# Performance work log

Hardware: AMD Instinct MI355X
Metric: run time of the kernel (lower is better)

## Reference

```python
import jax, jax.numpy as jnp
import numpy as np

N_NODES = 10000
N_EDGES = 160000
IN_CH = 1030
HID = 256
HEADS = 4
OUT_CH = 49
NEG_SLOPE = 0.2
EPS = 1e-5


def setup_inputs() -> dict:
    key = jax.random.key(0)
    ks = jax.random.split(key, 20)
    HC = HID * HEADS  # 1024
    inp = {
        "x": jax.random.normal(ks[0], (N_NODES, IN_CH), dtype=jnp.float32),
        "edge_index": jax.random.randint(ks[1], (2, N_EDGES), 0, N_NODES, dtype=jnp.int64),
        # conv1 (GATv2): lin_l (source), lin_r (target), att, out bias
        "c1_wl": jax.random.normal(ks[2], (IN_CH, HC), dtype=jnp.float32) * 0.03,
        "c1_bl": jnp.zeros((HC,), dtype=jnp.float32),
        "c1_wr": jax.random.normal(ks[3], (IN_CH, HC), dtype=jnp.float32) * 0.03,
        "c1_br": jnp.zeros((HC,), dtype=jnp.float32),
        "c1_att": jax.random.normal(ks[4], (HEADS, HID), dtype=jnp.float32) * 0.06,
        "c1_bias": jnp.zeros((HC,), dtype=jnp.float32),
        # norm1 (per-node LayerNorm over channels)
        "ln1_w": jnp.ones((HC,), dtype=jnp.float32),
        "ln1_b": jnp.zeros((HC,), dtype=jnp.float32),
        # conv2
        "c2_wl": jax.random.normal(ks[5], (HC, HC), dtype=jnp.float32) * 0.03,
        "c2_bl": jnp.zeros((HC,), dtype=jnp.float32),
        "c2_wr": jax.random.normal(ks[6], (HC, HC), dtype=jnp.float32) * 0.03,
        "c2_br": jnp.zeros((HC,), dtype=jnp.float32),
        "c2_att": jax.random.normal(ks[7], (HEADS, HID), dtype=jnp.float32) * 0.06,
        "c2_bias": jnp.zeros((HC,), dtype=jnp.float32),
        # norm2
        "ln2_w": jnp.ones((HC,), dtype=jnp.float32),
        "ln2_b": jnp.zeros((HC,), dtype=jnp.float32),
        # classifier: Linear(HC, HID) -> ELU -> Linear(HID, OUT_CH)
        "cls_w1": jax.random.normal(ks[8], (HC, HID), dtype=jnp.float32) * 0.03,
        "cls_b1": jnp.zeros((HID,), dtype=jnp.float32),
        "cls_w2": jax.random.normal(ks[9], (HID, OUT_CH), dtype=jnp.float32) * 0.06,
        "cls_b2": jnp.zeros((OUT_CH,), dtype=jnp.float32),
    }
    return inp


def gatv2_conv(x, src, dst, wl, bl, wr, br, att, bias, n_nodes):
    """PyG GATv2Conv, concat heads. src/dst include self loops."""
    H, C = att.shape
    xl = (x @ wl + bl).reshape(-1, H, C)  # source transform [N,H,C]
    xr = (x @ wr + br).reshape(-1, H, C)  # target transform [N,H,C]
    m = xl[src] + xr[dst]                  # [E,H,C] gather + add
    e = jnp.einsum("ehc,hc->eh", jax.nn.leaky_relu(m, NEG_SLOPE), att)  # [E,H]
    # segment softmax over destination node
    emax = jax.ops.segment_max(e, dst, num_segments=n_nodes)
    p = jnp.exp(e - emax[dst])
    denom = jax.ops.segment_sum(p, dst, num_segments=n_nodes)
    alpha = p / (denom[dst] + 1e-16)       # [E,H]
    out = jax.ops.segment_sum(xl[src] * alpha[:, :, None], dst, num_segments=n_nodes)
    return out.reshape(n_nodes, H * C) + bias


def layer_norm(x, w, b):
    mu = jnp.mean(x, axis=-1, keepdims=True)
    var = jnp.var(x, axis=-1, keepdims=True)
    return (x - mu) / jnp.sqrt(var + EPS) * w + b


def reference(x, edge_index, c1_wl, c1_bl, c1_wr, c1_br, c1_att, c1_bias,
              ln1_w, ln1_b, c2_wl, c2_bl, c2_wr, c2_br, c2_att, c2_bias,
              ln2_w, ln2_b, cls_w1, cls_b1, cls_w2, cls_b2):
    n = x.shape[0]
    loops = jnp.arange(n, dtype=edge_index.dtype)
    src = jnp.concatenate([edge_index[0], loops])  # add_self_loops=True
    dst = jnp.concatenate([edge_index[1], loops])

    h = gatv2_conv(x, src, dst, c1_wl, c1_bl, c1_wr, c1_br, c1_att, c1_bias, n)
    h = jax.nn.elu(layer_norm(h, ln1_w, ln1_b))
    # dropout: identity at inference
    h = gatv2_conv(h, src, dst, c2_wl, c2_bl, c2_wr, c2_br, c2_att, c2_bias, n)
    h = jax.nn.elu(layer_norm(h, ln2_w, ln2_b))
    h = jax.nn.elu(h @ cls_w1 + cls_b1)
    return h @ cls_w2 + cls_b2  # [N, 49]
```

## Files before the change

kernel.cpp:

```cpp
#include <hip/hip_runtime.h>
#include <stdint.h>

#define N_NODES 10000
#define N_EDGES 160000
#define E_TOT   170000
#define IN_CH   1030
#define HC      1024
#define OUT_CH  49
#define NEG_SLOPE 0.2f
#define LN_EPS 1e-5f
#define LOG2E 1.4426950408889634f

#define MPAD  10112
#define K1PAD 1088

typedef __attribute__((ext_vector_type(8))) __bf16 bf16x8;
typedef __attribute__((ext_vector_type(4))) float floatx4;
typedef __attribute__((ext_vector_type(2))) float floatx2;
typedef _Float16 h2 __attribute__((ext_vector_type(2)));

static __device__ __forceinline__ unsigned short f2bf(float f) {
  union { float f; uint32_t u; } v; v.f = f;
  uint32_t u = v.u;
  u += 0x7fffu + ((u >> 16) & 1u);
  return (unsigned short)(u >> 16);
}
static __device__ __forceinline__ unsigned short f2h(float f) {
  _Float16 h = (_Float16)f;
  union { _Float16 h; unsigned short u; } v; v.h = h; return v.u;
}
static __device__ __forceinline__ h2 bits2h2(uint32_t u) {
  union { uint32_t i; h2 h; } v; v.i = u; return v.h;
}
static __device__ __forceinline__ floatx2 h2f2(h2 a) {
  floatx2 r; r.x = (float)a.x; r.y = (float)a.y; return r;
}

static __device__ __forceinline__ float wred_add(float x) {
#define DPP_ADD(ctrl, rmask)                                                   \
  x += __builtin_bit_cast(float, __builtin_amdgcn_update_dpp(                  \
           0, __builtin_bit_cast(int, x), ctrl, rmask, 0xf, true))
  DPP_ADD(0x111, 0xf);
  DPP_ADD(0x112, 0xf);
  DPP_ADD(0x114, 0xf);
  DPP_ADD(0x118, 0xf);
  DPP_ADD(0x142, 0xa);
  DPP_ADD(0x143, 0xc);
#undef DPP_ADD
  return __builtin_bit_cast(float,
      __builtin_amdgcn_readlane(__builtin_bit_cast(int, x), 63));
}


__global__ void cast_x_kernel(const float* __restrict__ x, unsigned short* __restrict__ xa,
                              int* __restrict__ counts) {
  int idx = blockIdx.x * 256 + threadIdx.x;
  if (idx < N_NODES) counts[idx] = 0;
  if (idx >= N_NODES * K1PAD) return;
  int m = idx / K1PAD, k = idx - m * K1PAD;
  float v = (k < IN_CH) ? x[m * IN_CH + k] : 0.f;
  xa[idx] = f2bf(v);
}

static __device__ __forceinline__ void transpose_body(
    float (*tile)[33], const float* __restrict__ wa, const float* __restrict__ wb,
    int split, int lda, int ldb, int Kvalid, int Kout,
    unsigned short* __restrict__ out, int bx, int by, int t) {
  int n0 = bx * 32, k0 = by * 32;
  int tx = t & 31, ty = t >> 5;
#pragma unroll
  for (int i = 0; i < 4; i++) {
    int k = k0 + ty + i * 8;
    int n = n0 + tx;
    float v = 0.f;
    if (k < Kvalid) v = (n < split) ? wa[(size_t)k * lda + n] : wb[(size_t)k * ldb + (n - split)];
    tile[ty + i * 8][tx] = v;
  }
  __syncthreads();
#pragma unroll
  for (int i = 0; i < 4; i++) {
    int n = n0 + ty + i * 8;
    int k = k0 + tx;
    out[(size_t)n * Kout + k] = f2bf(tile[tx][ty + i * 8]);
  }
}

#define NB_W1 2176
#define NB_W2 2048
#define NB_WC 256
#define NB_CNT 665
__global__ __launch_bounds__(256) void prep2_kernel(
    const float* __restrict__ c1_wl, const float* __restrict__ c1_wr,
    const float* __restrict__ c2_wl, const float* __restrict__ c2_wr,
    const float* __restrict__ cls_w1,
    const int* __restrict__ dstArr, int* __restrict__ counts,
    unsigned short* __restrict__ wt1, unsigned short* __restrict__ wt2,
    unsigned short* __restrict__ wtc1)
{
  __shared__ float tile[32][33];
  int b = blockIdx.x, t = threadIdx.x;
  if (b < NB_W1) {
    transpose_body(tile, c1_wl, c1_wr, 1024, 1024, 1024, IN_CH, K1PAD, wt1, b & 63, b >> 6, t);
  } else if (b < NB_W1 + NB_W2) {
    int bb = b - NB_W1;
    transpose_body(tile, c2_wl, c2_wr, 1024, 1024, 1024, 1024, 1024, wt2, bb & 63, bb >> 6, t);
  } else if (b < NB_W1 + NB_W2 + NB_WC) {
    int bb = b - (NB_W1 + NB_W2);
    transpose_body(tile, cls_w1, cls_w1, 256, 256, 256, 1024, 1024, wtc1, bb & 7, bb >> 3, t);
  } else {
    int e = (b - (NB_W1 + NB_W2 + NB_WC)) * 256 + t;
    if (e < E_TOT) {
      int d = (e < N_EDGES) ? dstArr[e] : (e - N_EDGES);
      atomicAdd(&counts[d], 1);
    }
  }
}

__global__ __launch_bounds__(256) void scan_kernel(const int* __restrict__ counts,
                                                   int* __restrict__ rstart,
                                                   int* __restrict__ rwork) {
  __shared__ int sm[256];
  int t = threadIdx.x;
  int b0 = t * 40;
  int b1 = b0 + 40; if (b1 > N_NODES) b1 = N_NODES; if (b0 > N_NODES) b0 = N_NODES;
  int s = 0;
  for (int i = b0; i < b1; i++) s += counts[i];
  sm[t] = s; __syncthreads();
  for (int st = 1; st < 256; st <<= 1) {
    int add = (t >= st) ? sm[t - st] : 0;
    __syncthreads();
    sm[t] += add;
    __syncthreads();
  }
  int run = sm[t] - s;
  for (int i = b0; i < b1; i++) { rstart[i] = run; rwork[i] = run; run += counts[i]; }
  if (t == 255) rstart[N_NODES] = run;
}

__global__ void scatter_kernel(const int* __restrict__ srcArr, const int* __restrict__ dstArr,
                               int* __restrict__ rwork, int* __restrict__ csrsrc) {
  int e = blockIdx.x * 256 + threadIdx.x;
  if (e >= E_TOT) return;
  int d, sv;
  if (e < N_EDGES) { d = dstArr[e]; sv = srcArr[e]; }
  else { d = e - N_EDGES; sv = d; }
  int pos = atomicAdd(&rwork[d], 1);
  csrsrc[pos] = sv;
}

template <int MODE, int KC>
__global__ __launch_bounds__(256, 4) void gemm_bf16(
    const unsigned short* __restrict__ A, const unsigned short* __restrict__ Bt,
    float* __restrict__ Cf, unsigned short* __restrict__ Cb,
    const float* __restrict__ blo, const float* __restrict__ bhi,
    int M, int ldc, int bsplit)
{
  __shared__ __align__(16) unsigned short As[128 * 64];
  __shared__ __align__(16) unsigned short Bs[128 * 64];
  const int t = threadIdx.x;
  const int w = t >> 6, lane = t & 63;

  const unsigned int nwg = gridDim.x * gridDim.y;
  const unsigned int bid = blockIdx.y * gridDim.x + blockIdx.x;
  const unsigned int q8 = nwg >> 3, r8 = nwg & 7;
  const unsigned int xcd = bid & 7, sub = bid >> 3;
  const unsigned int wg = (xcd < r8 ? xcd * (q8 + 1) : r8 * (q8 + 1) + (xcd - r8) * q8) + sub;
  const int tile_n = (wg % gridDim.x) * 128, tile_m = (wg / gridDim.x) * 128;

  floatx4 acc[4][4] = {};

  const int qq = w * 64 + lane;
  const int row0 = qq >> 3;
  const int gj = (qq & 7) ^ (row0 & 7);
  const unsigned short* gA0 = A  + (size_t)(tile_m + row0) * KC + gj * 8;
  const unsigned short* gB0 = Bt + (size_t)(tile_n + row0) * KC + gj * 8;

  const int wm = (w >> 1) * 64, wn = (w & 1) * 64;
  const int lrow = lane & 15, cg0 = (lane >> 4);
  const int sw = lrow & 7;

#pragma unroll 1
  for (int k0 = 0; k0 < KC; k0 += 64) {
#pragma unroll
    for (int p = 0; p < 4; p++) {
      __builtin_amdgcn_global_load_lds(
          (const __attribute__((address_space(1))) void*)(gA0 + p * 32 * KC),
          (__attribute__((address_space(3))) void*)(As + p * 2048 + w * 512), 16, 0, 0);
      __builtin_amdgcn_global_load_lds(
          (const __attribute__((address_space(1))) void*)(gB0 + p * 32 * KC),
          (__attribute__((address_space(3))) void*)(Bs + p * 2048 + w * 512), 16, 0, 0);
    }
    gA0 += 64; gB0 += 64;
    __syncthreads();
#pragma unroll
    for (int h = 0; h < 2; h++) {
      const int sc = (h * 4 + cg0) ^ sw;
      bf16x8 a[4], b[4];
#pragma unroll
      for (int mi = 0; mi < 4; mi++)
        a[mi] = *(const bf16x8*)(As + (wm + mi * 16 + lrow) * 64 + sc * 8);
#pragma unroll
      for (int ni = 0; ni < 4; ni++)
        b[ni] = *(const bf16x8*)(Bs + (wn + ni * 16 + lrow) * 64 + sc * 8);
#pragma unroll
      for (int mi = 0; mi < 4; mi++)
#pragma unroll
        for (int ni = 0; ni < 4; ni++)
          acc[mi][ni] = __builtin_amdgcn_mfma_f32_16x16x32_bf16(a[mi], b[ni], acc[mi][ni], 0, 0, 0);
    }
    __syncthreads();
  }

  const int rbase = (lane >> 4) * 4;
#pragma unroll
  for (int mi = 0; mi < 4; mi++) {
#pragma unroll
    for (int r = 0; r < 4; r++) {
      int m = tile_m + wm + mi * 16 + rbase + r;
      if (m >= M) continue;
#pragma unroll
      for (int ni = 0; ni < 4; ni++) {
        int n = tile_n + wn + ni * 16 + lrow;
        float v = acc[mi][ni][r] + (n < bsplit ? blo[n] : bhi[n - bsplit]);
        if (MODE == 0) {
          Cf[(size_t)m * ldc + n] = v;
        } else if (MODE == 1) {
          Cf[(size_t)m * ldc + n] = v > 0.f ? v : expm1f(v);
        } else {
          Cb[(size_t)m * 2048 + n] = f2h(v);
        }
      }
    }
  }
}


__global__ __launch_bounds__(256) void gat_ln_kernel(
    const unsigned short* __restrict__ xlr,
    const float* __restrict__ att,
    const int* __restrict__ csrsrc, const int* __restrict__ rstart,
    const float* __restrict__ bias,
    const float* __restrict__ lnw, const float* __restrict__ lnb,
    unsigned short* __restrict__ out)
{
  const int d = blockIdx.x;
  const int t = threadIdx.x;
  const int lane = t & 63, wv = t >> 6;
  const int c = wv * 256 + lane * 4;

  uint2 xru = *(const uint2*)(xlr + (size_t)d * 2048 + 1024 + c);
  h2 xr0 = bits2h2(xru.x), xr1 = bits2h2(xru.y);
  float4 aw4 = *(const float4*)(att + c);
  h2 aw0, aw1;
  aw0.x = (_Float16)(aw4.x * LOG2E); aw0.y = (_Float16)(aw4.y * LOG2E);
  aw1.x = (_Float16)(aw4.z * LOG2E); aw1.y = (_Float16)(aw4.w * LOG2E);
  const h2 ns = {(_Float16)NEG_SLOPE, (_Float16)NEG_SLOPE};
  const unsigned short* xbase = xlr + c;

  const int start = rstart[d], end = rstart[d + 1];
  const int last = end - 1;
  const int ngroups = (end - start + 3) >> 2;

  float m = -3.0e38f, l = 0.f;
  floatx2 accA = {0.f, 0.f}, accB = {0.f, 0.f};

#define CIDX(e) csrsrc[(e) < last ? (e) : last]
  int sA0 = CIDX(start),     sA1 = CIDX(start + 1);
  int sA2 = CIDX(start + 2), sA3 = CIDX(start + 3);
  uint2 uA0 = *(const uint2*)(xbase + (size_t)sA0 * 2048);
  uint2 uA1 = *(const uint2*)(xbase + (size_t)sA1 * 2048);
  uint2 uA2 = *(const uint2*)(xbase + (size_t)sA2 * 2048);
  uint2 uA3 = *(const uint2*)(xbase + (size_t)sA3 * 2048);
  int sB0 = CIDX(start + 4), sB1 = CIDX(start + 5);
  int sB2 = CIDX(start + 6), sB3 = CIDX(start + 7);

  for (int g = 0; g < ngroups; g++) {
    const int base = start + (g << 2);
    int sC0 = CIDX(base + 8),  sC1 = CIDX(base + 9);
    int sC2 = CIDX(base + 10), sC3 = CIDX(base + 11);
    uint2 uB0 = *(const uint2*)(xbase + (size_t)sB0 * 2048);
    uint2 uB1 = *(const uint2*)(xbase + (size_t)sB1 * 2048);
    uint2 uB2 = *(const uint2*)(xbase + (size_t)sB2 * 2048);
    uint2 uB3 = *(const uint2*)(xbase + (size_t)sB3 * 2048);

    h2 xh0a = bits2h2(uA0.x), xh0b = bits2h2(uA0.y);
    h2 xh1a = bits2h2(uA1.x), xh1b = bits2h2(uA1.y);
    h2 xh2a = bits2h2(uA2.x), xh2b = bits2h2(uA2.y);
    h2 xh3a = bits2h2(uA3.x), xh3b = bits2h2(uA3.y);
    h2 t0a = xh0a + xr0, t0b = xh0b + xr1;
    h2 t1a = xh1a + xr0, t1b = xh1b + xr1;
    h2 t2a = xh2a + xr0, t2b = xh2b + xr1;
    h2 t3a = xh3a + xr0, t3b = xh3b + xr1;
    h2 r0a = __builtin_elementwise_max(t0a, t0a * ns);
    h2 r0b = __builtin_elementwise_max(t0b, t0b * ns);
    h2 r1a = __builtin_elementwise_max(t1a, t1a * ns);
    h2 r1b = __builtin_elementwise_max(t1b, t1b * ns);
    h2 r2a = __builtin_elementwise_max(t2a, t2a * ns);
    h2 r2b = __builtin_elementwise_max(t2b, t2b * ns);
    h2 r3a = __builtin_elementwise_max(t3a, t3a * ns);
    h2 r3b = __builtin_elementwise_max(t3b, t3b * ns);
    float p0 = __builtin_amdgcn_fdot2(r0b, aw1, __builtin_amdgcn_fdot2(r0a, aw0, 0.f, false), false);
    float p1 = __builtin_amdgcn_fdot2(r1b, aw1, __builtin_amdgcn_fdot2(r1a, aw0, 0.f, false), false);
    float p2 = __builtin_amdgcn_fdot2(r2b, aw1, __builtin_amdgcn_fdot2(r2a, aw0, 0.f, false), false);
    float p3 = __builtin_amdgcn_fdot2(r3b, aw1, __builtin_amdgcn_fdot2(r3a, aw0, 0.f, false), false);
    p0 = wred_add(p0);
    p1 = wred_add(p1);
    p2 = wred_add(p2);
    p3 = wred_add(p3);
    float mx = fmaxf(fmaxf(p0, p1), fmaxf(p2, p3));
    if (mx > m) {
      float sc = exp2f(m - mx);
      floatx2 scv; scv.x = sc; scv.y = sc;
      accA *= scv; accB *= scv; l *= sc;
      m = mx;
    }
    float pe0 = exp2f(p0 - m);
    float pe1 = (base + 1 <= last) ? exp2f(p1 - m) : 0.f;
    float pe2 = (base + 2 <= last) ? exp2f(p2 - m) : 0.f;
    float pe3 = (base + 3 <= last) ? exp2f(p3 - m) : 0.f;
    floatx2 x0A = h2f2(xh0a), x0B = h2f2(xh0b);
    floatx2 x1A = h2f2(xh1a), x1B = h2f2(xh1b);
    floatx2 x2A = h2f2(xh2a), x2B = h2f2(xh2b);
    floatx2 x3A = h2f2(xh3a), x3B = h2f2(xh3b);
    floatx2 v0; v0.x = pe0; v0.y = pe0;
    floatx2 v1; v1.x = pe1; v1.y = pe1;
    floatx2 v2; v2.x = pe2; v2.y = pe2;
    floatx2 v3; v3.x = pe3; v3.y = pe3;
    accA += x0A * v0; accA += x1A * v1; accA += x2A * v2; accA += x3A * v3;
    accB += x0B * v0; accB += x1B * v1; accB += x2B * v2; accB += x3B * v3;
    l += pe0 + pe1 + pe2 + pe3;

    uA0 = uB0; uA1 = uB1; uA2 = uB2; uA3 = uB3;
    sB0 = sC0; sB1 = sC1; sB2 = sC2; sB3 = sC3;
  }
#undef CIDX

  float rd = 1.f / (l + 1e-16f);
  float4 bv = *(const float4*)(bias + c);
  float o0 = accA.x * rd + bv.x, o1 = accA.y * rd + bv.y;
  float o2 = accB.x * rd + bv.z, o3 = accB.y * rd + bv.w;

  __shared__ float ws1[4], ws2[4];
  float s1 = o0 + o1 + o2 + o3;
  float s2 = o0 * o0 + o1 * o1 + o2 * o2 + o3 * o3;
#pragma unroll
  for (int mm = 32; mm >= 1; mm >>= 1) {
    s1 += __shfl_xor(s1, mm, 64);
    s2 += __shfl_xor(s2, mm, 64);
  }
  if (lane == 0) { ws1[wv] = s1; ws2[wv] = s2; }
  __syncthreads();
  float mean = (ws1[0] + ws1[1] + ws1[2] + ws1[3]) * (1.f / 1024.f);
  float var  = (ws2[0] + ws2[1] + ws2[2] + ws2[3]) * (1.f / 1024.f) - mean * mean;
  float rstd = rsqrtf(var + LN_EPS);
  float4 wv4 = *(const float4*)(lnw + c);
  float4 bb  = *(const float4*)(lnb + c);
  float z0 = (o0 - mean) * rstd * wv4.x + bb.x; z0 = z0 > 0.f ? z0 : expm1f(z0);
  float z1 = (o1 - mean) * rstd * wv4.y + bb.y; z1 = z1 > 0.f ? z1 : expm1f(z1);
  float z2 = (o2 - mean) * rstd * wv4.z + bb.z; z2 = z2 > 0.f ? z2 : expm1f(z2);
  float z3 = (o3 - mean) * rstd * wv4.w + bb.w; z3 = z3 > 0.f ? z3 : expm1f(z3);
  ushort4 u;
  u.x = f2bf(z0); u.y = f2bf(z1); u.z = f2bf(z2); u.w = f2bf(z3);
  *(ushort4*)(out + (size_t)d * 1024 + c) = u;
}


__global__ __launch_bounds__(64) void cls2_kernel(
    const float* __restrict__ h3, const float* __restrict__ w2,
    const float* __restrict__ b2, float* __restrict__ out)
{
  __shared__ float row[256];
  int node = blockIdx.x, t = threadIdx.x;
  *(float4*)(row + t * 4) = *(const float4*)(h3 + (size_t)node * 256 + t * 4);
  __syncthreads();
  if (t < OUT_CH) {
    float a0 = 0.f, a1 = 0.f, a2 = 0.f, a3 = 0.f;
#pragma unroll 4
    for (int k = 0; k < 256; k += 4) {
      float4 r = *(const float4*)(row + k);
      a0 += r.x * w2[(k + 0) * OUT_CH + t];
      a1 += r.y * w2[(k + 1) * OUT_CH + t];
      a2 += r.z * w2[(k + 2) * OUT_CH + t];
      a3 += r.w * w2[(k + 3) * OUT_CH + t];
    }
    out[node * OUT_CH + t] = (a0 + a1) + (a2 + a3) + b2[t];
  }
}


extern "C" void kernel_launch(void* const* d_in, const int* in_sizes, int n_in,
                              void* d_out, int out_size, void* d_ws, size_t ws_size,
                              hipStream_t stream)
{
  const float* x       = (const float*)d_in[0];
  const int*   ei      = (const int*)d_in[1];
  const float* c1_wl   = (const float*)d_in[2];
  const float* c1_bl   = (const float*)d_in[3];
  const float* c1_wr   = (const float*)d_in[4];
  const float* c1_br   = (const float*)d_in[5];
  const float* c1_att  = (const float*)d_in[6];
  const float* c1_bias = (const float*)d_in[7];
  const float* ln1_w   = (const float*)d_in[8];
  const float* ln1_b   = (const float*)d_in[9];
  const float* c2_wl   = (const float*)d_in[10];
  const float* c2_bl   = (const float*)d_in[11];
  const float* c2_wr   = (const float*)d_in[12];
  const float* c2_br   = (const float*)d_in[13];
  const float* c2_att  = (const float*)d_in[14];
  const float* c2_bias = (const float*)d_in[15];
  const float* ln2_w   = (const float*)d_in[16];
  const float* ln2_b   = (const float*)d_in[17];
  const float* cls_w1  = (const float*)d_in[18];
  const float* cls_b1  = (const float*)d_in[19];
  const float* cls_w2  = (const float*)d_in[20];
  const float* cls_b2  = (const float*)d_in[21];

  const int* srcArr = ei;
  const int* dstArr = ei + N_EDGES;

  char* ws = (char*)d_ws;
  size_t off = 0;
  auto alloc = [&](size_t bytes) { void* p = ws + off; off += (bytes + 255) & ~(size_t)255; return p; };
  unsigned short* xa      = (unsigned short*)alloc((size_t)MPAD * K1PAD * 2);
  unsigned short* wt1     = (unsigned short*)alloc((size_t)2048 * K1PAD * 2);
  unsigned short* wt2     = (unsigned short*)alloc((size_t)2048 * 1024 * 2);
  unsigned short* wtc1    = (unsigned short*)alloc((size_t)256 * 1024 * 2);
  unsigned short* xlr     = (unsigned short*)alloc((size_t)N_NODES * 2048 * 2);
  float*          h3      = (float*)alloc((size_t)N_NODES * 256 * 4);
  unsigned short* hb      = (unsigned short*)alloc((size_t)MPAD * 1024 * 2);
  int*            counts  = (int*)alloc(N_NODES * 4);
  int*            rwork   = (int*)alloc(N_NODES * 4);
  int*            rstart  = (int*)alloc((N_NODES + 1) * 4);
  int*            csrsrc  = (int*)alloc(E_TOT * 4);
  (void)in_sizes; (void)n_in; (void)out_size; (void)ws_size;

  cast_x_kernel<<<(N_NODES * K1PAD + 255) / 256, 256, 0, stream>>>(x, xa, counts);
  prep2_kernel<<<NB_W1 + NB_W2 + NB_WC + NB_CNT, 256, 0, stream>>>(
      c1_wl, c1_wr, c2_wl, c2_wr, cls_w1, dstArr, counts, wt1, wt2, wtc1);

  scan_kernel<<<1, 256, 0, stream>>>(counts, rstart, rwork);
  scatter_kernel<<<(E_TOT + 255) / 256, 256, 0, stream>>>(srcArr, dstArr, rwork, csrsrc);

  gemm_bf16<2, K1PAD><<<dim3(16, 79), 256, 0, stream>>>(xa, wt1, nullptr, xlr, c1_bl, c1_br, N_NODES, 0, 1024);
  gat_ln_kernel<<<N_NODES, 256, 0, stream>>>(xlr, c1_att, csrsrc, rstart, c1_bias, ln1_w, ln1_b, hb);

  gemm_bf16<2, 1024><<<dim3(16, 79), 256, 0, stream>>>(hb, wt2, nullptr, xlr, c2_bl, c2_br, N_NODES, 0, 1024);
  gat_ln_kernel<<<N_NODES, 256, 0, stream>>>(xlr, c2_att, csrsrc, rstart, c2_bias, ln2_w, ln2_b, hb);

  gemm_bf16<1, 1024><<<dim3(2, 79), 256, 0, stream>>>(hb, wtc1, h3, nullptr, cls_b1, cls_b1, N_NODES, 256, 1024);
  cls2_kernel<<<N_NODES, 64, 0, stream>>>(h3, cls_w2, cls_b2, (float*)d_out);
}
```

Measured before the change: 498.3 us.

## Split GAT edge loop into two independent online-softmax streams with deeper prefetch

The per-node GATv2 aggregation loop now interleaves two independent groups of four edges, each with its own running max, sum and accumulators, merged after the loop. Leftover edges are handled by a scalar tail loop. The CSR index array is padded with zeros so prefetch reads past the end stay in bounds without clamping. The intent is to double the gathers in flight and shorten the dependency chain through the softmax rescale. The cost is more registers, a merge step, and wasted gather loads for padded or out-of-range prefetches.

```diff
diff --git a/kernel.cpp b/kernel.cpp
--- a/kernel.cpp
+++ b/kernel.cpp
@@ -49,6 +49,57 @@
 #undef DPP_ADD
   return __builtin_bit_cast(float,
       __builtin_amdgcn_readlane(__builtin_bit_cast(int, x), 63));
+}
+
+static __device__ __forceinline__ void group4(
+    uint2 u0, uint2 u1, uint2 u2, uint2 u3,
+    h2 xr0, h2 xr1, h2 aw0, h2 aw1, h2 ns,
+    float& m, float& l, floatx2& acc0, floatx2& acc1)
+{
+  h2 xh0a = bits2h2(u0.x), xh0b = bits2h2(u0.y);
+  h2 xh1a = bits2h2(u1.x), xh1b = bits2h2(u1.y);
+  h2 xh2a = bits2h2(u2.x), xh2b = bits2h2(u2.y);
+  h2 xh3a = bits2h2(u3.x), xh3b = bits2h2(u3.y);
+  h2 t0a = xh0a + xr0, t0b = xh0b + xr1;
+  h2 t1a = xh1a + xr0, t1b = xh1b + xr1;
+  h2 t2a = xh2a + xr0, t2b = xh2b + xr1;
+  h2 t3a = xh3a + xr0, t3b = xh3b + xr1;
+  h2 r0a = __builtin_elementwise_max(t0a, t0a * ns);
+  h2 r0b = __builtin_elementwise_max(t0b, t0b * ns);
+  h2 r1a = __builtin_elementwise_max(t1a, t1a * ns);
+  h2 r1b = __builtin_elementwise_max(t1b, t1b * ns);
+  h2 r2a = __builtin_elementwise_max(t2a, t2a * ns);
+  h2 r2b = __builtin_elementwise_max(t2b, t2b * ns);
+  h2 r3a = __builtin_elementwise_max(t3a, t3a * ns);
+  h2 r3b = __builtin_elementwise_max(t3b, t3b * ns);
+  float p0 = __builtin_amdgcn_fdot2(r0b, aw1, __builtin_amdgcn_fdot2(r0a, aw0, 0.f, false), false);
+  float p1 = __builtin_amdgcn_fdot2(r1b, aw1, __builtin_amdgcn_fdot2(r1a, aw0, 0.f, false), false);
+  float p2 = __builtin_amdgcn_fdot2(r2b, aw1, __builtin_amdgcn_fdot2(r2a, aw0, 0.f, false), false);
+  float p3 = __builtin_amdgcn_fdot2(r3b, aw1, __builtin_amdgcn_fdot2(r3a, aw0, 0.f, false), false);
+  p0 = wred_add(p0);
+  p1 = wred_add(p1);
+  p2 = wred_add(p2);
+  p3 = wred_add(p3);
+  float mx = fmaxf(fmaxf(p0, p1), fmaxf(p2, p3));
+  if (mx > m) {
+    float sc = exp2f(m - mx);
+    floatx2 scv; scv.x = sc; scv.y = sc;
+    acc0 *= scv; acc1 *= scv; l *= sc;
+    m = mx;
+  }
+  float pe0 = exp2f(p0 - m), pe1 = exp2f(p1 - m);
+  float pe2 = exp2f(p2 - m), pe3 = exp2f(p3 - m);
+  floatx2 x0A = h2f2(xh0a), x0B = h2f2(xh0b);
+  floatx2 x1A = h2f2(xh1a), x1B = h2f2(xh1b);
+  floatx2 x2A = h2f2(xh2a), x2B = h2f2(xh2b);
+  floatx2 x3A = h2f2(xh3a), x3B = h2f2(xh3b);
+  floatx2 v0; v0.x = pe0; v0.y = pe0;
+  floatx2 v1; v1.x = pe1; v1.y = pe1;
+  floatx2 v2; v2.x = pe2; v2.y = pe2;
+  floatx2 v3; v3.x = pe3; v3.y = pe3;
+  acc0 += x0A * v0; acc0 += x1A * v1; acc0 += x2A * v2; acc0 += x3A * v3;
+  acc1 += x0B * v0; acc1 += x1B * v1; acc1 += x2B * v2; acc1 += x3B * v3;
+  l += pe0 + pe1 + pe2 + pe3;
 }
 
 
@@ -141,6 +192,7 @@
                                int* __restrict__ rwork, int* __restrict__ csrsrc) {
   int e = blockIdx.x * 256 + threadIdx.x;
   if (e >= E_TOT) return;
+  if (e < 32) csrsrc[E_TOT + e] = 0;
   int d, sv;
   if (e < N_EDGES) { d = dstArr[e]; sv = srcArr[e]; }
   else { d = e - N_EDGES; sv = d; }
@@ -258,82 +310,79 @@
   const unsigned short* xbase = xlr + c;
 
   const int start = rstart[d], end = rstart[d + 1];
-  const int last = end - 1;
-  const int ngroups = (end - start + 3) >> 2;
-
-  float m = -3.0e38f, l = 0.f;
-  floatx2 accA = {0.f, 0.f}, accB = {0.f, 0.f};
-
-#define CIDX(e) csrsrc[(e) < last ? (e) : last]
-  int sA0 = CIDX(start),     sA1 = CIDX(start + 1);
-  int sA2 = CIDX(start + 2), sA3 = CIDX(start + 3);
-  uint2 uA0 = *(const uint2*)(xbase + (size_t)sA0 * 2048);
-  uint2 uA1 = *(const uint2*)(xbase + (size_t)sA1 * 2048);
-  uint2 uA2 = *(const uint2*)(xbase + (size_t)sA2 * 2048);
-  uint2 uA3 = *(const uint2*)(xbase + (size_t)sA3 * 2048);
-  int sB0 = CIDX(start + 4), sB1 = CIDX(start + 5);
-  int sB2 = CIDX(start + 6), sB3 = CIDX(start + 7);
-
-  for (int g = 0; g < ngroups; g++) {
-    const int base = start + (g << 2);
-    int sC0 = CIDX(base + 8),  sC1 = CIDX(base + 9);
-    int sC2 = CIDX(base + 10), sC3 = CIDX(base + 11);
-    uint2 uB0 = *(const uint2*)(xbase + (size_t)sB0 * 2048);
-    uint2 uB1 = *(const uint2*)(xbase + (size_t)sB1 * 2048);
-    uint2 uB2 = *(const uint2*)(xbase + (size_t)sB2 * 2048);
-    uint2 uB3 = *(const uint2*)(xbase + (size_t)sB3 * 2048);
-
-    h2 xh0a = bits2h2(uA0.x), xh0b = bits2h2(uA0.y);
-    h2 xh1a = bits2h2(uA1.x), xh1b = bits2h2(uA1.y);
-    h2 xh2a = bits2h2(uA2.x), xh2b = bits2h2(uA2.y);
-    h2 xh3a = bits2h2(uA3.x), xh3b = bits2h2(uA3.y);
+  const int ng = (end - start) >> 2;
+  const int nA = (ng + 1) >> 1, nB = ng >> 1;
+
+  float mA = -3.0e38f, lA = 0.f, mB = -3.0e38f, lB = 0.f;
+  floatx2 a0A = {0.f, 0.f}, a1A = {0.f, 0.f};
+  floatx2 a0B = {0.f, 0.f}, a1B = {0.f, 0.f};
+
+  int iA0 = csrsrc[start],     iA1 = csrsrc[start + 1];
+  int iA2 = csrsrc[start + 2], iA3 = csrsrc[start + 3];
+  int iB0 = csrsrc[start + 4], iB1 = csrsrc[start + 5];
+  int iB2 = csrsrc[start + 6], iB3 = csrsrc[start + 7];
+  uint2 uA0 = *(const uint2*)(xbase + (size_t)iA0 * 2048);
+  uint2 uA1 = *(const uint2*)(xbase + (size_t)iA1 * 2048);
+  uint2 uA2 = *(const uint2*)(xbase + (size_t)iA2 * 2048);
+  uint2 uA3 = *(const uint2*)(xbase + (size_t)iA3 * 2048);
+  uint2 uB0 = *(const uint2*)(xbase + (size_t)iB0 * 2048);
+  uint2 uB1 = *(const uint2*)(xbase + (size_t)iB1 * 2048);
+  uint2 uB2 = *(const uint2*)(xbase + (size_t)iB2 * 2048);
+  uint2 uB3 = *(const uint2*)(xbase + (size_t)iB3 * 2048);
+  iA0 = csrsrc[start + 8];  iA1 = csrsrc[start + 9];
+  iA2 = csrsrc[start + 10]; iA3 = csrsrc[start + 11];
+  iB0 = csrsrc[start + 12]; iB1 = csrsrc[start + 13];
+  iB2 = csrsrc[start + 14]; iB3 = csrsrc[start + 15];
+
+  for (int j = 0; j < nA; j++) {
+    const int base = start + (j << 3);
+    group4(uA0, uA1, uA2, uA3, xr0, xr1, aw0, aw1, ns, mA, lA, a0A, a1A);
+    uA0 = *(const uint2*)(xbase + (size_t)iA0 * 2048);
+    uA1 = *(const uint2*)(xbase + (size_t)iA1 * 2048);
+    uA2 = *(const uint2*)(xbase + (size_t)iA2 * 2048);
+    uA3 = *(const uint2*)(xbase + (size_t)iA3 * 2048);
+    iA0 = csrsrc[base + 16]; iA1 = csrsrc[base + 17];
+    iA2 = csrsrc[base + 18]; iA3 = csrsrc[base + 19];
+    if (j < nB)
+      group4(uB0, uB1, uB2, uB3, xr0, xr1, aw0, aw1, ns, mB, lB, a0B, a1B);
+    uB0 = *(const uint2*)(xbase + (size_t)iB0 * 2048);
+    uB1 = *(const uint2*)(xbase + (size_t)iB1 * 2048);
+    uB2 = *(const uint2*)(xbase + (size_t)iB2 * 2048);
+    uB3 = *(const uint2*)(xbase + (size_t)iB3 * 2048);
+    iB0 = csrsrc[base + 20]; iB1 = csrsrc[base + 21];
+    iB2 = csrsrc[base + 22]; iB3 = csrsrc[base + 23];
+  }
+
+  float m = fmaxf(mA, mB);
+  float sA = exp2f(mA - m), sB = exp2f(mB - m);
+  float l = lA * sA + lB * sB;
+  floatx2 vsA; vsA.x = sA; vsA.y = sA;
+  floatx2 vsB; vsB.x = sB; vsB.y = sB;
+  floatx2 accA = a0A * vsA + a0B * vsB;
+  floatx2 accB = a1A * vsA + a1B * vsB;
+
+  for (int i = start + (ng << 2); i < end; i++) {
+    int s0 = csrsrc[i];
+    uint2 u0 = *(const uint2*)(xbase + (size_t)s0 * 2048);
+    h2 xh0a = bits2h2(u0.x), xh0b = bits2h2(u0.y);
     h2 t0a = xh0a + xr0, t0b = xh0b + xr1;
-    h2 t1a = xh1a + xr0, t1b = xh1b + xr1;
-    h2 t2a = xh2a + xr0, t2b = xh2b + xr1;
-    h2 t3a = xh3a + xr0, t3b = xh3b + xr1;
     h2 r0a = __builtin_elementwise_max(t0a, t0a * ns);
     h2 r0b = __builtin_elementwise_max(t0b, t0b * ns);
-    h2 r1a = __builtin_elementwise_max(t1a, t1a * ns);
-    h2 r1b = __builtin_elementwise_max(t1b, t1b * ns);
-    h2 r2a = __builtin_elementwise_max(t2a, t2a * ns);
-    h2 r2b = __builtin_elementwise_max(t2b, t2b * ns);
-    h2 r3a = __builtin_elementwise_max(t3a, t3a * ns);
-    h2 r3b = __builtin_elementwise_max(t3b, t3b * ns);
     float p0 = __builtin_amdgcn_fdot2(r0b, aw1, __builtin_amdgcn_fdot2(r0a, aw0, 0.f, false), false);
-    float p1 = __builtin_amdgcn_fdot2(r1b, aw1, __builtin_amdgcn_fdot2(r1a, aw0, 0.f, false), false);
-    float p2 = __builtin_amdgcn_fdot2(r2b, aw1, __builtin_amdgcn_fdot2(r2a, aw0, 0.f, false), false);
-    float p3 = __builtin_amdgcn_fdot2(r3b, aw1, __builtin_amdgcn_fdot2(r3a, aw0, 0.f, false), false);
     p0 = wred_add(p0);
-    p1 = wred_add(p1);
-    p2 = wred_add(p2);
-    p3 = wred_add(p3);
-    float mx = fmaxf(fmaxf(p0, p1), fmaxf(p2, p3));
-    if (mx > m) {
-      float sc = exp2f(m - mx);
+    if (p0 > m) {
+      float sc = exp2f(m - p0);
       floatx2 scv; scv.x = sc; scv.y = sc;
       accA *= scv; accB *= scv; l *= sc;
-      m = mx;
+      m = p0;
     }
     float pe0 = exp2f(p0 - m);
-    float pe1 = (base + 1 <= last) ? exp2f(p1 - m) : 0.f;
-    float pe2 = (base + 2 <= last) ? exp2f(p2 - m) : 0.f;
-    float pe3 = (base + 3 <= last) ? exp2f(p3 - m) : 0.f;
     floatx2 x0A = h2f2(xh0a), x0B = h2f2(xh0b);
-    floatx2 x1A = h2f2(xh1a), x1B = h2f2(xh1b);
-    floatx2 x2A = h2f2(xh2a), x2B = h2f2(xh2b);
-    floatx2 x3A = h2f2(xh3a), x3B = h2f2(xh3b);
-    floatx2 v0; v0.x = pe0; v0.y = pe0;
-    floatx2 v1; v1.x = pe1; v1.y = pe1;
-    floatx2 v2; v2.x = pe2; v2.y = pe2;
-    floatx2 v3; v3.x = pe3; v3.y = pe3;
-    accA += x0A * v0; accA += x1A * v1; accA += x2A * v2; accA += x3A * v3;
-    accB += x0B * v0; accB += x1B * v1; accB += x2B * v2; accB += x3B * v3;
-    l += pe0 + pe1 + pe2 + pe3;
-
-    uA0 = uB0; uA1 = uB1; uA2 = uB2; uA3 = uB3;
-    sB0 = sC0; sB1 = sC1; sB2 = sC2; sB3 = sC3;
-  }
-#undef CIDX
+    floatx2 pe0v; pe0v.x = pe0; pe0v.y = pe0;
+    accA += x0A * pe0v;
+    accB += x0B * pe0v;
+    l += pe0;
+  }
 
   float rd = 1.f / (l + 1e-16f);
   float4 bv = *(const float4*)(bias + c);
@@ -431,7 +480,7 @@
   int*            counts  = (int*)alloc(N_NODES * 4);
   int*            rwork   = (int*)alloc(N_NODES * 4);
   int*            rstart  = (int*)alloc((N_NODES + 1) * 4);
-  int*            csrsrc  = (int*)alloc(E_TOT * 4);
+  int*            csrsrc  = (int*)alloc((E_TOT + 32) * 4);
   (void)in_sizes; (void)n_in; (void)out_size; (void)ws_size;
 
   cast_x_kernel<<<(N_NODES * K1PAD + 255) / 256, 256, 0, stream>>>(x, xa, counts);
```

Result: no change. 507.3 us (+1.8%).

## Split GAT aggregation per head with head-major layout and separate LayerNorm kernel

Applied to the files above, without the earlier changes.

The GEMM epilogue now writes xl and xr into separate head-major buffers ([head][node][256]). The aggregation kernel is restructured so each block handles one head for four nodes, one node per wave, with the block index swizzled so nearby blocks share a head. Each head's gathered source rows then sit in a compact 5 MB region, which is meant to improve L2 locality for the random neighbor gathers. LayerNorm+ELU moves to a separate kernel that reads an intermediate fp16 buffer, adding one extra launch and a round trip of 20 MB.

```diff
diff --git a/kernel.cpp b/kernel.cpp
--- a/kernel.cpp
+++ b/kernel.cpp
@@ -141,6 +141,7 @@
                                int* __restrict__ rwork, int* __restrict__ csrsrc) {
   int e = blockIdx.x * 256 + threadIdx.x;
   if (e >= E_TOT) return;
+  if (e < 32) csrsrc[E_TOT + e] = 0;
   int d, sv;
   if (e < N_EDGES) { d = dstArr[e]; sv = srcArr[e]; }
   else { d = e - N_EDGES; sv = d; }
@@ -152,6 +153,7 @@
 __global__ __launch_bounds__(256, 4) void gemm_bf16(
     const unsigned short* __restrict__ A, const unsigned short* __restrict__ Bt,
     float* __restrict__ Cf, unsigned short* __restrict__ Cb,
+    unsigned short* __restrict__ Cb2,
     const float* __restrict__ blo, const float* __restrict__ bhi,
     int M, int ldc, int bsplit)
 {
@@ -227,7 +229,9 @@
         } else if (MODE == 1) {
           Cf[(size_t)m * ldc + n] = v > 0.f ? v : expm1f(v);
         } else {
-          Cb[(size_t)m * 2048 + n] = f2h(v);
+          unsigned short* dst = (n < 1024) ? Cb : Cb2;
+          int hh = (n >> 8) & 3, ch = n & 255;
+          dst[((size_t)hh * N_NODES + m) * 256 + ch] = f2h(v);
         }
       }
     }
@@ -235,110 +239,151 @@
 }
 
 
-__global__ __launch_bounds__(256) void gat_ln_kernel(
-    const unsigned short* __restrict__ xlr,
+__global__ __launch_bounds__(256) void gat_head_kernel(
+    const unsigned short* __restrict__ xlh,
+    const unsigned short* __restrict__ xrh,
     const float* __restrict__ att,
     const int* __restrict__ csrsrc, const int* __restrict__ rstart,
     const float* __restrict__ bias,
+    unsigned short* __restrict__ obuf)
+{
+  const int bid = blockIdx.x;
+  const int h = (bid & 7) >> 1;
+  const int g = ((bid >> 3) << 1) | (bid & 1);
+  const int t = threadIdx.x;
+  const int lane = t & 63, wv = t >> 6;
+  const int d = g * 4 + wv;
+  const int c = lane * 4;
+  const size_t hoff = (size_t)h * (N_NODES * 256);
+
+  uint2 xru = *(const uint2*)(xrh + hoff + (size_t)d * 256 + c);
+  h2 xr0 = bits2h2(xru.x), xr1 = bits2h2(xru.y);
+  float4 aw4 = *(const float4*)(att + h * 256 + c);
+  h2 aw0, aw1;
+  aw0.x = (_Float16)(aw4.x * LOG2E); aw0.y = (_Float16)(aw4.y * LOG2E);
+  aw1.x = (_Float16)(aw4.z * LOG2E); aw1.y = (_Float16)(aw4.w * LOG2E);
+  const h2 ns = {(_Float16)NEG_SLOPE, (_Float16)NEG_SLOPE};
+  const unsigned short* xbase = xlh + hoff + c;
+
+  int start = rstart[d], deg = rstart[d + 1] - start;
+
+  float m = -3.0e38f, l = 0.f;
+  floatx2 accA = {0.f, 0.f}, accB = {0.f, 0.f};
+
+  int i = 0;
+  if (deg >= 4) {
+    int sA0 = csrsrc[start],     sA1 = csrsrc[start + 1];
+    int sA2 = csrsrc[start + 2], sA3 = csrsrc[start + 3];
+    uint2 uA0 = *(const uint2*)(xbase + (size_t)sA0 * 256);
+    uint2 uA1 = *(const uint2*)(xbase + (size_t)sA1 * 256);
+    uint2 uA2 = *(const uint2*)(xbase + (size_t)sA2 * 256);
+    uint2 uA3 = *(const uint2*)(xbase + (size_t)sA3 * 256);
+    int sB0 = csrsrc[start + 4], sB1 = csrsrc[start + 5];
+    int sB2 = csrsrc[start + 6], sB3 = csrsrc[start + 7];
+    for (; i + 4 <= deg; i += 4) {
+      int sC0 = csrsrc[start + i + 8],  sC1 = csrsrc[start + i + 9];
+      int sC2 = csrsrc[start + i + 10], sC3 = csrsrc[start + i + 11];
+      uint2 uB0 = *(const uint2*)(xbase + (size_t)sB0 * 256);
+      uint2 uB1 = *(const uint2*)(xbase + (size_t)sB1 * 256);
+      uint2 uB2 = *(const uint2*)(xbase + (size_t)sB2 * 256);
+      uint2 uB3 = *(const uint2*)(xbase + (size_t)sB3 * 256);
+
+      h2 xh0a = bits2h2(uA0.x), xh0b = bits2h2(uA0.y);
+      h2 xh1a = bits2h2(uA1.x), xh1b = bits2h2(uA1.y);
+      h2 xh2a = bits2h2(uA2.x), xh2b = bits2h2(uA2.y);
+      h2 xh3a = bits2h2(uA3.x), xh3b = bits2h2(uA3.y);
+      h2 t0a = xh0a + xr0, t0b = xh0b + xr1;
+      h2 t1a = xh1a + xr0, t1b = xh1b + xr1;
+      h2 t2a = xh2a + xr0, t2b = xh2b + xr1;
+      h2 t3a = xh3a + xr0, t3b = xh3b + xr1;
+      h2 r0a = __builtin_elementwise_max(t0a, t0a * ns);
+      h2 r0b = __builtin_elementwise_max(t0b, t0b * ns);
+      h2 r1a = __builtin_elementwise_max(t1a, t1a * ns);
+      h2 r1b = __builtin_elementwise_max(t1b, t1b * ns);
+      h2 r2a = __builtin_elementwise_max(t2a, t2a * ns);
+      h2 r2b = __builtin_elementwise_max(t2b, t2b * ns);
+      h2 r3a = __builtin_elementwise_max(t3a, t3a * ns);
+      h2 r3b = __builtin_elementwise_max(t3b, t3b * ns);
+      float p0 = __builtin_amdgcn_fdot2(r0b, aw1, __builtin_amdgcn_fdot2(r0a, aw0, 0.f, false), false);
+      float p1 = __builtin_amdgcn_fdot2(r1b, aw1, __builtin_amdgcn_fdot2(r1a, aw0, 0.f, false), false);
+      float p2 = __builtin_amdgcn_fdot2(r2b, aw1, __builtin_amdgcn_fdot2(r2a, aw0, 0.f, false), false);
+      float p3 = __builtin_amdgcn_fdot2(r3b, aw1, __builtin_amdgcn_fdot2(r3a, aw0, 0.f, false), false);
+      p0 = wred_add(p0);
+      p1 = wred_add(p1);
+      p2 = wred_add(p2);
+      p3 = wred_add(p3);
+      float mx = fmaxf(fmaxf(p0, p1), fmaxf(p2, p3));
+      if (mx > m) {
+        float sc = exp2f(m - mx);
+        floatx2 scv; scv.x = sc; scv.y = sc;
+        accA *= scv; accB *= scv; l *= sc;
+        m = mx;
+      }
+      float pe0 = exp2f(p0 - m), pe1 = exp2f(p1 - m);
+      float pe2 = exp2f(p2 - m), pe3 = exp2f(p3 - m);
+      floatx2 x0A = h2f2(xh0a), x0B = h2f2(xh0b);
+      floatx2 x1A = h2f2(xh1a), x1B = h2f2(xh1b);
+      floatx2 x2A = h2f2(xh2a), x2B = h2f2(xh2b);
+      floatx2 x3A = h2f2(xh3a), x3B = h2f2(xh3b);
+      floatx2 v0; v0.x = pe0; v0.y = pe0;
+      floatx2 v1; v1.x = pe1; v1.y = pe1;
+      floatx2 v2; v2.x = pe2; v2.y = pe2;
+      floatx2 v3; v3.x = pe3; v3.y = pe3;
+      accA += x0A * v0; accA += x1A * v1; accA += x2A * v2; accA += x3A * v3;
+      accB += x0B * v0; accB += x1B * v1; accB += x2B * v2; accB += x3B * v3;
+      l += pe0 + pe1 + pe2 + pe3;
+
+      uA0 = uB0; uA1 = uB1; uA2 = uB2; uA3 = uB3;
+      sB0 = sC0; sB1 = sC1; sB2 = sC2; sB3 = sC3;
+    }
+  }
+  for (; i < deg; i++) {
+    int s0 = csrsrc[start + i];
+    uint2 u0 = *(const uint2*)(xbase + (size_t)s0 * 256);
+    h2 xh0a = bits2h2(u0.x), xh0b = bits2h2(u0.y);
+    h2 t0a = xh0a + xr0, t0b = xh0b + xr1;
+    h2 r0a = __builtin_elementwise_max(t0a, t0a * ns);
+    h2 r0b = __builtin_elementwise_max(t0b, t0b * ns);
+    float p0 = __builtin_amdgcn_fdot2(r0b, aw1, __builtin_amdgcn_fdot2(r0a, aw0, 0.f, false), false);
+    p0 = wred_add(p0);
+    if (p0 > m) {
+      float sc = exp2f(m - p0);
+      floatx2 scv; scv.x = sc; scv.y = sc;
+      accA *= scv; accB *= scv; l *= sc;
+      m = p0;
+    }
+    float pe0 = exp2f(p0 - m);
+    floatx2 x0A = h2f2(xh0a), x0B = h2f2(xh0b);
+    floatx2 pe0v; pe0v.x = pe0; pe0v.y = pe0;
+    accA += x0A * pe0v;
+    accB += x0B * pe0v;
+    l += pe0;
+  }
+
+  float rd = 1.f / (l + 1e-16f);
+  float4 bv = *(const float4*)(bias + h * 256 + c);
+  float o0 = accA.x * rd + bv.x, o1 = accA.y * rd + bv.y;
+  float o2 = accB.x * rd + bv.z, o3 = accB.y * rd + bv.w;
+  ushort4 u;
+  u.x = f2h(o0); u.y = f2h(o1); u.z = f2h(o2); u.w = f2h(o3);
+  *(ushort4*)(obuf + hoff + (size_t)d * 256 + c) = u;
+}
+
+
+__global__ __launch_bounds__(256) void ln_elu_kernel(
+    const unsigned short* __restrict__ obuf,
     const float* __restrict__ lnw, const float* __restrict__ lnb,
     unsigned short* __restrict__ out)
 {
   const int d = blockIdx.x;
   const int t = threadIdx.x;
   const int lane = t & 63, wv = t >> 6;
-  const int c = wv * 256 + lane * 4;
-
-  uint2 xru = *(const uint2*)(xlr + (size_t)d * 2048 + 1024 + c);
-  h2 xr0 = bits2h2(xru.x), xr1 = bits2h2(xru.y);
-  float4 aw4 = *(const float4*)(att + c);
-  h2 aw0, aw1;
-  aw0.x = (_Float16)(aw4.x * LOG2E); aw0.y = (_Float16)(aw4.y * LOG2E);
-  aw1.x = (_Float16)(aw4.z * LOG2E); aw1.y = (_Float16)(aw4.w * LOG2E);
-  const h2 ns = {(_Float16)NEG_SLOPE, (_Float16)NEG_SLOPE};
-  const unsigned short* xbase = xlr + c;
-
-  const int start = rstart[d], end = rstart[d + 1];
-  const int last = end - 1;
-  const int ngroups = (end - start + 3) >> 2;
-
-  float m = -3.0e38f, l = 0.f;
-  floatx2 accA = {0.f, 0.f}, accB = {0.f, 0.f};
-
-#define CIDX(e) csrsrc[(e) < last ? (e) : last]
-  int sA0 = CIDX(start),     sA1 = CIDX(start + 1);
-  int sA2 = CIDX(start + 2), sA3 = CIDX(start + 3);
-  uint2 uA0 = *(const uint2*)(xbase + (size_t)sA0 * 2048);
-  uint2 uA1 = *(const uint2*)(xbase + (size_t)sA1 * 2048);
-  uint2 uA2 = *(const uint2*)(xbase + (size_t)sA2 * 2048);
-  uint2 uA3 = *(const uint2*)(xbase + (size_t)sA3 * 2048);
-  int sB0 = CIDX(start + 4), sB1 = CIDX(start + 5);
-  int sB2 = CIDX(start + 6), sB3 = CIDX(start + 7);
-
-  for (int g = 0; g < ngroups; g++) {
-    const int base = start + (g << 2);
-    int sC0 = CIDX(base + 8),  sC1 = CIDX(base + 9);
-    int sC2 = CIDX(base + 10), sC3 = CIDX(base + 11);
-    uint2 uB0 = *(const uint2*)(xbase + (size_t)sB0 * 2048);
-    uint2 uB1 = *(const uint2*)(xbase + (size_t)sB1 * 2048);
-    uint2 uB2 = *(const uint2*)(xbase + (size_t)sB2 * 2048);
-    uint2 uB3 = *(const uint2*)(xbase + (size_t)sB3 * 2048);
-
-    h2 xh0a = bits2h2(uA0.x), xh0b = bits2h2(uA0.y);
-    h2 xh1a = bits2h2(uA1.x), xh1b = bits2h2(uA1.y);
-    h2 xh2a = bits2h2(uA2.x), xh2b = bits2h2(uA2.y);
-    h2 xh3a = bits2h2(uA3.x), xh3b = bits2h2(uA3.y);
-    h2 t0a = xh0a + xr0, t0b = xh0b + xr1;
-    h2 t1a = xh1a + xr0, t1b = xh1b + xr1;
-    h2 t2a = xh2a + xr0, t2b = xh2b + xr1;
-    h2 t3a = xh3a + xr0, t3b = xh3b + xr1;
-    h2 r0a = __builtin_elementwise_max(t0a, t0a * ns);
-    h2 r0b = __builtin_elementwise_max(t0b, t0b * ns);
-    h2 r1a = __builtin_elementwise_max(t1a, t1a * ns);
-    h2 r1b = __builtin_elementwise_max(t1b, t1b * ns);
-    h2 r2a = __builtin_elementwise_max(t2a, t2a * ns);
-    h2 r2b = __builtin_elementwise_max(t2b, t2b * ns);
-    h2 r3a = __builtin_elementwise_max(t3a, t3a * ns);
-    h2 r3b = __builtin_elementwise_max(t3b, t3b * ns);
-    float p0 = __builtin_amdgcn_fdot2(r0b, aw1, __builtin_amdgcn_fdot2(r0a, aw0, 0.f, false), false);
-    float p1 = __builtin_amdgcn_fdot2(r1b, aw1, __builtin_amdgcn_fdot2(r1a, aw0, 0.f, false), false);
-    float p2 = __builtin_amdgcn_fdot2(r2b, aw1, __builtin_amdgcn_fdot2(r2a, aw0, 0.f, false), false);
-    float p3 = __builtin_amdgcn_fdot2(r3b, aw1, __builtin_amdgcn_fdot2(r3a, aw0, 0.f, false), false);
-    p0 = wred_add(p0);
-    p1 = wred_add(p1);
-    p2 = wred_add(p2);
-    p3 = wred_add(p3);
-    float mx = fmaxf(fmaxf(p0, p1), fmaxf(p2, p3));
-    if (mx > m) {
-      float sc = exp2f(m - mx);
-      floatx2 scv; scv.x = sc; scv.y = sc;
-      accA *= scv; accB *= scv; l *= sc;
-      m = mx;
-    }
-    float pe0 = exp2f(p0 - m);
-    float pe1 = (base + 1 <= last) ? exp2f(p1 - m) : 0.f;
-    float pe2 = (base + 2 <= last) ? exp2f(p2 - m) : 0.f;
-    float pe3 = (base + 3 <= last) ? exp2f(p3 - m) : 0.f;
-    floatx2 x0A = h2f2(xh0a), x0B = h2f2(xh0b);
-    floatx2 x1A = h2f2(xh1a), x1B = h2f2(xh1b);
-    floatx2 x2A = h2f2(xh2a), x2B = h2f2(xh2b);
-    floatx2 x3A = h2f2(xh3a), x3B = h2f2(xh3b);
-    floatx2 v0; v0.x = pe0; v0.y = pe0;
-    floatx2 v1; v1.x = pe1; v1.y = pe1;
-    floatx2 v2; v2.x = pe2; v2.y = pe2;
-    floatx2 v3; v3.x = pe3; v3.y = pe3;
-    accA += x0A * v0; accA += x1A * v1; accA += x2A * v2; accA += x3A * v3;
-    accB += x0B * v0; accB += x1B * v1; accB += x2B * v2; accB += x3B * v3;
-    l += pe0 + pe1 + pe2 + pe3;
-
-    uA0 = uB0; uA1 = uB1; uA2 = uB2; uA3 = uB3;
-    sB0 = sC0; sB1 = sC1; sB2 = sC2; sB3 = sC3;
-  }
-#undef CIDX
-
-  float rd = 1.f / (l + 1e-16f);
-  float4 bv = *(const float4*)(bias + c);
-  float o0 = accA.x * rd + bv.x, o1 = accA.y * rd + bv.y;
-  float o2 = accB.x * rd + bv.z, o3 = accB.y * rd + bv.w;
+  const int ch = lane * 4;
+  const int c = wv * 256 + ch;
+
+  uint2 ov = *(const uint2*)(obuf + ((size_t)wv * N_NODES + d) * 256 + ch);
+  h2 oa = bits2h2(ov.x), ob = bits2h2(ov.y);
+  float o0 = (float)oa.x, o1 = (float)oa.y, o2 = (float)ob.x, o3 = (float)ob.y;
 
   __shared__ float ws1[4], ws2[4];
   float s1 = o0 + o1 + o2 + o3;
@@ -425,13 +470,15 @@
   unsigned short* wt1     = (unsigned short*)alloc((size_t)2048 * K1PAD * 2);
   unsigned short* wt2     = (unsigned short*)alloc((size_t)2048 * 1024 * 2);
   unsigned short* wtc1    = (unsigned short*)alloc((size_t)256 * 1024 * 2);
-  unsigned short* xlr     = (unsigned short*)alloc((size_t)N_NODES * 2048 * 2);
+  unsigned short* xlh     = (unsigned short*)alloc((size_t)4 * N_NODES * 256 * 2);
+  unsigned short* xrh     = (unsigned short*)alloc((size_t)4 * N_NODES * 256 * 2);
+  unsigned short* obuf    = (unsigned short*)alloc((size_t)4 * N_NODES * 256 * 2);
   float*          h3      = (float*)alloc((size_t)N_NODES * 256 * 4);
   unsigned short* hb      = (unsigned short*)alloc((size_t)MPAD * 1024 * 2);
   int*            counts  = (int*)alloc(N_NODES * 4);
   int*            rwork   = (int*)alloc(N_NODES * 4);
   int*            rstart  = (int*)alloc((N_NODES + 1) * 4);
-  int*            csrsrc  = (int*)alloc(E_TOT * 4);
+  int*            csrsrc  = (int*)alloc((E_TOT + 32) * 4);
   (void)in_sizes; (void)n_in; (void)out_size; (void)ws_size;
 
   cast_x_kernel<<<(N_NODES * K1PAD + 255) / 256, 256, 0, stream>>>(x, xa, counts);
@@ -441,12 +488,14 @@
   scan_kernel<<<1, 256, 0, stream>>>(counts, rstart, rwork);
   scatter_kernel<<<(E_TOT + 255) / 256, 256, 0, stream>>>(srcArr, dstArr, rwork, csrsrc);
 
-  gemm_bf16<2, K1PAD><<<dim3(16, 79), 256, 0, stream>>>(xa, wt1, nullptr, xlr, c1_bl, c1_br, N_NODES, 0, 1024);
-  gat_ln_kernel<<<N_NODES, 256, 0, stream>>>(xlr, c1_att, csrsrc, rstart, c1_bias, ln1_w, ln1_b, hb);
-
-  gemm_bf16<2, 1024><<<dim3(16, 79), 256, 0, stream>>>(hb, wt2, nullptr, xlr, c2_bl, c2_br, N_NODES, 0, 1024);
-  gat_ln_kernel<<<N_NODES, 256, 0, stream>>>(xlr, c2_att, csrsrc, rstart, c2_bias, ln2_w, ln2_b, hb);
-
-  gemm_bf16<1, 1024><<<dim3(2, 79), 256, 0, stream>>>(hb, wtc1, h3, nullptr, cls_b1, cls_b1, N_NODES, 256, 1024);
+  gemm_bf16<2, K1PAD><<<dim3(16, 79), 256, 0, stream>>>(xa, wt1, nullptr, xlh, xrh, c1_bl, c1_br, N_NODES, 0, 1024);
+  gat_head_kernel<<<N_NODES, 256, 0, stream>>>(xlh, xrh, c1_att, csrsrc, rstart, c1_bias, obuf);
+  ln_elu_kernel<<<N_NODES, 256, 0, stream>>>(obuf, ln1_w, ln1_b, hb);
+
+  gemm_bf16<2, 1024><<<dim3(16, 79), 256, 0, stream>>>(hb, wt2, nullptr, xlh, xrh, c2_bl, c2_br, N_NODES, 0, 1024);
+  gat_head_kernel<<<N_NODES, 256, 0, stream>>>(xlh, xrh, c2_att, csrsrc, rstart, c2_bias, obuf);
+  ln_elu_kernel<<<N_NODES, 256, 0, stream>>>(obuf, ln2_w, ln2_b, hb);
+
+  gemm_bf16<1, 1024><<<dim3(2, 79), 256, 0, stream>>>(hb, wtc1, h3, nullptr, nullptr, cls_b1, cls_b1, N_NODES, 256, 1024);
   cls2_kernel<<<N_NODES, 64, 0, stream>>>(h3, cls_w2, cls_b2, (float*)d_out);
 }
```

Result: slower. 514.6 us (+3.3%).
